# Kernel optimization log

Hardware: AMD Instinct MI355X
Metric: run time of the kernel (lower is better)

Reference implementation:

```python
import jax, jax.numpy as jnp
import numpy as np

N_NODES = 100000
N_EDGES = 1250000
IN_CH = 128
OUT_CH = 64


def setup_inputs() -> dict:
    key = jax.random.key(0)
    k1, k2, k3, k4 = jax.random.split(key, 4)
    x = jax.random.normal(k1, (N_NODES, IN_CH), dtype=jnp.float32)
    edge_index = jax.random.randint(k2, (2, N_EDGES), 0, N_NODES, dtype=jnp.int64)
    edge_weight = jax.random.uniform(k3, (N_EDGES,), dtype=jnp.float32)
    # Xavier-uniform weight, zero bias (as in reset_parameters)
    limit = float(np.sqrt(6.0 / (IN_CH + OUT_CH)))
    W = jax.random.uniform(k4, (IN_CH, OUT_CH), dtype=jnp.float32, minval=-limit, maxval=limit)
    b = jnp.zeros((OUT_CH,), dtype=jnp.float32)
    return {"x": x, "edge_index": edge_index, "edge_weight": edge_weight, "W": W, "b": b}


def reference(x, edge_index, edge_weight, W, b):
    # Dense transform: [N, in] @ [in, out] -> [N, out]
    h = jnp.matmul(x, W)
    row, col = edge_index[0], edge_index[1]
    n = h.shape[0]
    # Weighted in-degree via scatter-add on destination (row)
    deg = jnp.zeros((n,), dtype=h.dtype).at[row].add(edge_weight)
    # deg^-0.5 with inf (deg==0) replaced by 0
    deg_inv_sqrt = jnp.where(deg == 0, jnp.zeros_like(deg), deg ** -0.5)
    norm = deg_inv_sqrt[row] * deg_inv_sqrt[col]  # [E]
    # Gather source features, normalize, scatter-add to destinations
    out = jnp.zeros_like(h).at[row].add(h[col] * norm[:, None])
    return out + b
```

## Files before the change

kernel.cpp:

```cpp
#include <hip/hip_runtime.h>

#define N_NODES 100000
#define N_EDGES 1250000
#define IN_CH 128
#define OUT_CH 64

#define NPB 128
#define ACCS2 33
#define NBINS 782
#define BINCAP_DEF 2048
#define NB1 256
#define B1T 512
#define CH1 ((N_EDGES + NB1 - 1) / NB1)
#define MAXU ((CH1 + B1T - 1) / B1T)
#define CURS_STRIDE 16

#define QSCALE 8192.0f
#define QBIAS_F 16777216.0f
#define QBIAS_U 16777216u
#define INV_QSCALE 1.220703125e-4f
#define SCALE_DEG 33554432.0f
#define INV_SCALE_DEG 2.9802322387695312e-08f

typedef __attribute__((ext_vector_type(8))) short short8;
typedef __attribute__((ext_vector_type(4))) float f32x4;

__device__ inline unsigned int f2bf(float f) {
    unsigned int u = __float_as_uint(f);
    unsigned int r = ((u >> 16) & 1u) + 0x7FFFu;
    return (u + r) >> 16;
}
__device__ inline float bf_lo(unsigned int p) { return __uint_as_float(p << 16); }
__device__ inline float bf_hi(unsigned int p) { return __uint_as_float(p & 0xFFFF0000u); }

__device__ inline unsigned long long qpack(unsigned int p) {
    unsigned int lo = (unsigned int)__float2int_rn(fmaf(bf_lo(p), QSCALE, QBIAS_F));
    unsigned int hi = (unsigned int)__float2int_rn(fmaf(bf_hi(p), QSCALE, QBIAS_F));
    return ((unsigned long long)hi << 32) | (unsigned long long)lo;
}

__global__ __launch_bounds__(256) void wbconv_kernel(const float* __restrict__ W,
                                                     unsigned int* __restrict__ Wb,
                                                     int* __restrict__ cursor,
                                                     int bincap) {
    int g = blockIdx.x * 256 + threadIdx.x;
    if (g < NBINS) cursor[g * CURS_STRIDE] = g * bincap;

    int c = g >> 8;
    int t = (g >> 6) & 3;
    int l = g & 63;
    int q = l >> 4, r15 = l & 15;
    unsigned int o[4];
#pragma unroll
    for (int jj = 0; jj < 4; ++jj) {
        float f0 = W[(c * 32 + q * 8 + 2 * jj)     * OUT_CH + t * 16 + r15];
        float f1 = W[(c * 32 + q * 8 + 2 * jj + 1) * OUT_CH + t * 16 + r15];
        o[jj] = f2bf(f0) | (f2bf(f1) << 16);
    }
    *(uint4*)(Wb + (size_t)g * 4) = make_uint4(o[0], o[1], o[2], o[3]);
}

__global__ __launch_bounds__(B1T) void bin1_kernel(const int* __restrict__ ei,
                                                   const float* __restrict__ ew,
                                                   int* __restrict__ cursor,
                                                   int2* __restrict__ brec,
                                                   int bincap) {
    __shared__ int hist[NBINS];
    __shared__ int base[NBINS];
    __shared__ int rank[NBINS];
    const int t = threadIdx.x;
    for (int i = t; i < NBINS; i += B1T) { hist[i] = 0; rank[i] = 0; }
    __syncthreads();

    const int e0 = blockIdx.x * CH1;
    const int e1 = (e0 + CH1 < N_EDGES) ? e0 + CH1 : N_EDGES;

    int rowv[MAXU], colv[MAXU];
    float wv[MAXU];
#pragma unroll
    for (int u = 0; u < MAXU; ++u) {
        int e = e0 + t + u * B1T;
        bool ok = e < e1;
        rowv[u] = ok ? ei[e] : -1;
        colv[u] = ok ? ei[N_EDGES + e] : 0;
        wv[u]   = ok ? ew[e] : 0.0f;
        if (ok) atomicAdd(&hist[rowv[u] >> 7], 1);
    }
    __syncthreads();

    for (int i = t; i < NBINS; i += B1T)
        if (hist[i] > 0) base[i] = atomicAdd(&cursor[i * CURS_STRIDE], hist[i]);
    __syncthreads();

#pragma unroll
    for (int u = 0; u < MAXU; ++u) {
        if (rowv[u] >= 0) {
            int b = rowv[u] >> 7;
            int rk = atomicAdd(&rank[b], 1);
            int idx = base[b] + rk;
            if (idx < (b + 1) * bincap)
                brec[idx] = make_int2(((rowv[u] & 127) << 17) | colv[u],
                                      __float_as_int(wv[u]));
        }
    }
}

__global__ __launch_bounds__(256) void bin2_kernel(const int* __restrict__ cursor,
                                                   const int2* __restrict__ brec,
                                                   float* __restrict__ dis_g,
                                                   int bincap) {
    __shared__ int deg[NPB];
    const int t = threadIdx.x;
    const int b = blockIdx.x;
    if (t < NPB) deg[t] = 0;
    __syncthreads();

    const int rbase = b * bincap;
    int m = cursor[b * CURS_STRIDE] - rbase;
    if (m > bincap) m = bincap;

    for (int j = t; j < m; j += 256) {
        int2 rec = brec[rbase + j];
        atomicAdd(&deg[rec.x >> 17], __float2int_rn(__int_as_float(rec.y) * SCALE_DEG));
    }
    __syncthreads();

    int node = b * NPB + t;
    if (t < NPB && node < N_NODES) {
        float d = (float)deg[t] * INV_SCALE_DEG;
        dis_g[node] = (d == 0.0f) ? 0.0f : (1.0f / sqrtf(d));
    }
}

__global__ __launch_bounds__(256) void gemm_kernel(const float* __restrict__ x,
                                                   const unsigned int* __restrict__ Wb,
                                                   const float* __restrict__ dis,
                                                   unsigned int* __restrict__ hs) {
    const int tid  = threadIdx.x;
    const int w    = tid >> 6;
    const int lane = tid & 63;
    const int q    = lane >> 4, r15 = lane & 15;
    const int node = blockIdx.x * 64 + w * 16 + r15;
    const int nl   = (node < N_NODES) ? node : N_NODES - 1;
    const float* xrow = x + (size_t)nl * IN_CH;

    f32x4 acc[4];
#pragma unroll
    for (int t = 0; t < 4; ++t) acc[t] = (f32x4){0.f, 0.f, 0.f, 0.f};

#pragma unroll
    for (int c = 0; c < 4; ++c) {
        float4 xa = *(const float4*)(xrow + c * 32 + q * 8);
        float4 xb = *(const float4*)(xrow + c * 32 + q * 8 + 4);
        short8 bfrag;
        bfrag[0] = (short)f2bf(xa.x); bfrag[1] = (short)f2bf(xa.y);
        bfrag[2] = (short)f2bf(xa.z); bfrag[3] = (short)f2bf(xa.w);
        bfrag[4] = (short)f2bf(xb.x); bfrag[5] = (short)f2bf(xb.y);
        bfrag[6] = (short)f2bf(xb.z); bfrag[7] = (short)f2bf(xb.w);
#pragma unroll
        for (int t = 0; t < 4; ++t) {
            short8 afrag = *(const short8*)(Wb + (size_t)((c * 4 + t) * 64 + lane) * 4);
            acc[t] = __builtin_amdgcn_mfma_f32_16x16x32_bf16(afrag, bfrag, acc[t], 0, 0, 0);
        }
    }

    if (node < N_NODES) {
        float di = dis[node];
#pragma unroll
        for (int t = 0; t < 4; ++t) {
            unsigned int p0 = f2bf(acc[t][0] * di) | (f2bf(acc[t][1] * di) << 16);
            unsigned int p1 = f2bf(acc[t][2] * di) | (f2bf(acc[t][3] * di) << 16);
            *(uint2*)(hs + (size_t)node * 32 + t * 8 + q * 2) = make_uint2(p0, p1);
        }
    }
}

__global__ __launch_bounds__(512) void bingather_kernel(const int* __restrict__ cursor,
                                                        const int2* __restrict__ brec,
                                                        const uint4* __restrict__ hs,
                                                        const float* __restrict__ dis,
                                                        const float* __restrict__ b,
                                                        float* __restrict__ out,
                                                        int bincap) {
    __shared__ unsigned long long acc[NPB * ACCS2];
    __shared__ int cnt[NPB];
    const int t = threadIdx.x;
    const int blk = blockIdx.x;
    for (int k = t; k < NPB * ACCS2; k += 512) acc[k] = 0ull;
    if (t < NPB) cnt[t] = 0;
    __syncthreads();

    const int rbase = blk * bincap;
    int m = cursor[blk * CURS_STRIDE] - rbase;
    if (m > bincap) m = bincap;

    const int wid = t >> 6, lane = t & 63;
    const int sub = lane >> 3, l8 = lane & 7;

    for (int j0 = wid * 16; j0 < m; j0 += 128) {
        int jA = j0 + sub;
        int jB = j0 + 8 + sub;
        bool okA = jA < m, okB = jB < m;
        int recA = okA ? brec[rbase + jA].x : 0;
        int recB = okB ? brec[rbase + jB].x : 0;
        uint4 pA = make_uint4(0, 0, 0, 0), pB = make_uint4(0, 0, 0, 0);
        if (okA) pA = hs[(size_t)(recA & 0x1FFFF) * 8 + l8];
        if (okB) pB = hs[(size_t)(recB & 0x1FFFF) * 8 + l8];
        if (okA) {
            int ba = (recA >> 17) * ACCS2 + 4 * l8;
            atomicAdd(&acc[ba + 0], qpack(pA.x));
            atomicAdd(&acc[ba + 1], qpack(pA.y));
            atomicAdd(&acc[ba + 2], qpack(pA.z));
            atomicAdd(&acc[ba + 3], qpack(pA.w));
            if (l8 == 0) atomicAdd(&cnt[recA >> 17], 1);
        }
        if (okB) {
            int bb = (recB >> 17) * ACCS2 + 4 * l8;
            atomicAdd(&acc[bb + 0], qpack(pB.x));
            atomicAdd(&acc[bb + 1], qpack(pB.y));
            atomicAdd(&acc[bb + 2], qpack(pB.z));
            atomicAdd(&acc[bb + 3], qpack(pB.w));
            if (l8 == 0) atomicAdd(&cnt[recB >> 17], 1);
        }
    }
    __syncthreads();

    const unsigned int* acc32 = (const unsigned int*)acc;
    float bc = b[lane];
    int half = lane & 1, slot = lane >> 1;
#pragma unroll 4
    for (int r = 0; r < 16; ++r) {
        int nl = wid * 16 + r;
        int node = blk * NPB + nl;
        if (node < N_NODES) {
            unsigned int raw = acc32[(nl * ACCS2 + slot) * 2 + half];
            int qsum = (int)(raw - (unsigned int)cnt[nl] * QBIAS_U);
            float di = dis[node] * INV_QSCALE;
            out[(size_t)node * OUT_CH + lane] = (float)qsum * di + bc;
        }
    }
}

extern "C" void kernel_launch(void* const* d_in, const int* in_sizes, int n_in,
                              void* d_out, int out_size, void* d_ws, size_t ws_size,
                              hipStream_t stream) {
    const float* x  = (const float*)d_in[0];
    const int*   ei = (const int*)d_in[1];
    const float* ew = (const float*)d_in[2];
    const float* W  = (const float*)d_in[3];
    const float* b  = (const float*)d_in[4];
    float* out = (float*)d_out;

    unsigned int* hs = (unsigned int*)d_ws;
    unsigned int* Wb = hs + (size_t)N_NODES * 32;
    int*   cursor  = (int*)(Wb + 4096);
    float* dis     = (float*)(cursor + NBINS * CURS_STRIDE);
    int2*  brec    = (int2*)(dis + N_NODES);
    size_t used = (size_t)N_NODES * 32 + 4096 + (size_t)NBINS * CURS_STRIDE
                + (size_t)N_NODES;
    size_t rem  = (ws_size / 4 > used) ? ws_size / 4 - used : 0;
    int bincap  = (int)(rem / (2 * (size_t)NBINS));
    if (bincap > BINCAP_DEF) bincap = BINCAP_DEF;

    wbconv_kernel<<<4, 256, 0, stream>>>(W, Wb, cursor, bincap);
    bin1_kernel<<<NB1, B1T, 0, stream>>>(ei, ew, cursor, brec, bincap);
    bin2_kernel<<<NBINS, 256, 0, stream>>>(cursor, brec, dis, bincap);
    gemm_kernel<<<(N_NODES + 63) / 64, 256, 0, stream>>>(x, Wb, dis, hs);
    bingather_kernel<<<NBINS, 512, 0, stream>>>(cursor, brec, (const uint4*)hs,
                                                dis, b, out, bincap);
}
```

Measured before the change: 164.5 us.

## Fuse binning and GEMM into one launch, compute degree via global atomics

Merges the edge-binning pass and the dense bf16 MFMA transform into one kernel, with separate blocks doing each job so they run concurrently. The separate degree kernel is dropped: weighted degree is accumulated with global integer atomics during binning, and the source-side normalisation moves into the gather, where each edge looks up the source degree and takes rsqrt. Edge records shrink from 8 to 4 bytes because the weight is no longer stored, and the quantisation bias is halved. The trade is many global atomics on the degree array plus an extra degree load and rsqrt per edge in the gather.

```diff
diff --git a/kernel.cpp b/kernel.cpp
--- a/kernel.cpp
+++ b/kernel.cpp
@@ -14,10 +14,11 @@
 #define CH1 ((N_EDGES + NB1 - 1) / NB1)
 #define MAXU ((CH1 + B1T - 1) / B1T)
 #define CURS_STRIDE 16
+#define GEMM_BLOCKS ((N_NODES + 127) / 128)
 
 #define QSCALE 8192.0f
-#define QBIAS_F 16777216.0f
-#define QBIAS_U 16777216u
+#define QBIAS_F 8388608.0f
+#define QBIAS_U 8388608u
 #define INV_QSCALE 1.220703125e-4f
 #define SCALE_DEG 33554432.0f
 #define INV_SCALE_DEG 2.9802322387695312e-08f
@@ -33,193 +34,175 @@
 __device__ inline float bf_lo(unsigned int p) { return __uint_as_float(p << 16); }
 __device__ inline float bf_hi(unsigned int p) { return __uint_as_float(p & 0xFFFF0000u); }
 
-__device__ inline unsigned long long qpack(unsigned int p) {
-    unsigned int lo = (unsigned int)__float2int_rn(fmaf(bf_lo(p), QSCALE, QBIAS_F));
-    unsigned int hi = (unsigned int)__float2int_rn(fmaf(bf_hi(p), QSCALE, QBIAS_F));
+__device__ inline unsigned long long qpacks(unsigned int p, float sc) {
+    unsigned int lo = (unsigned int)__float2int_rn(fmaf(bf_lo(p), sc, QBIAS_F));
+    unsigned int hi = (unsigned int)__float2int_rn(fmaf(bf_hi(p), sc, QBIAS_F));
     return ((unsigned long long)hi << 32) | (unsigned long long)lo;
 }
 
-__global__ __launch_bounds__(256) void wbconv_kernel(const float* __restrict__ W,
-                                                     unsigned int* __restrict__ Wb,
-                                                     int* __restrict__ cursor,
-                                                     int bincap) {
+__global__ __launch_bounds__(256) void init_kernel(const float* __restrict__ W,
+                                                   unsigned int* __restrict__ Wb,
+                                                   int* __restrict__ cursor,
+                                                   int* __restrict__ deg,
+                                                   int bincap) {
     int g = blockIdx.x * 256 + threadIdx.x;
     if (g < NBINS) cursor[g * CURS_STRIDE] = g * bincap;
-
-    int c = g >> 8;
-    int t = (g >> 6) & 3;
-    int l = g & 63;
-    int q = l >> 4, r15 = l & 15;
-    unsigned int o[4];
-#pragma unroll
-    for (int jj = 0; jj < 4; ++jj) {
-        float f0 = W[(c * 32 + q * 8 + 2 * jj)     * OUT_CH + t * 16 + r15];
-        float f1 = W[(c * 32 + q * 8 + 2 * jj + 1) * OUT_CH + t * 16 + r15];
-        o[jj] = f2bf(f0) | (f2bf(f1) << 16);
-    }
-    *(uint4*)(Wb + (size_t)g * 4) = make_uint4(o[0], o[1], o[2], o[3]);
-}
-
-__global__ __launch_bounds__(B1T) void bin1_kernel(const int* __restrict__ ei,
-                                                   const float* __restrict__ ew,
-                                                   int* __restrict__ cursor,
-                                                   int2* __restrict__ brec,
-                                                   int bincap) {
+    if (g < 25000) *(uint4*)(deg + g * 4) = make_uint4(0u, 0u, 0u, 0u);
+    if (g < 1024) {
+        int c = g >> 8;
+        int t4 = (g >> 6) & 3;
+        int l = g & 63;
+        int q = l >> 4, r15 = l & 15;
+        unsigned int o[4];
+#pragma unroll
+        for (int jj = 0; jj < 4; ++jj) {
+            float f0 = W[(c * 32 + q * 8 + 2 * jj)     * OUT_CH + t4 * 16 + r15];
+            float f1 = W[(c * 32 + q * 8 + 2 * jj + 1) * OUT_CH + t4 * 16 + r15];
+            o[jj] = f2bf(f0) | (f2bf(f1) << 16);
+        }
+        *(uint4*)(Wb + (size_t)g * 4) = make_uint4(o[0], o[1], o[2], o[3]);
+    }
+}
+
+__global__ __launch_bounds__(512) void fused_kernel(const float* __restrict__ x,
+                                                    const unsigned int* __restrict__ Wb,
+                                                    const int* __restrict__ ei,
+                                                    const float* __restrict__ ew,
+                                                    int* __restrict__ cursor,
+                                                    int* __restrict__ deg,
+                                                    int* __restrict__ brec,
+                                                    unsigned int* __restrict__ hs,
+                                                    int bincap) {
     __shared__ int hist[NBINS];
     __shared__ int base[NBINS];
     __shared__ int rank[NBINS];
-    const int t = threadIdx.x;
-    for (int i = t; i < NBINS; i += B1T) { hist[i] = 0; rank[i] = 0; }
-    __syncthreads();
-
-    const int e0 = blockIdx.x * CH1;
-    const int e1 = (e0 + CH1 < N_EDGES) ? e0 + CH1 : N_EDGES;
-
-    int rowv[MAXU], colv[MAXU];
-    float wv[MAXU];
-#pragma unroll
-    for (int u = 0; u < MAXU; ++u) {
-        int e = e0 + t + u * B1T;
-        bool ok = e < e1;
-        rowv[u] = ok ? ei[e] : -1;
-        colv[u] = ok ? ei[N_EDGES + e] : 0;
-        wv[u]   = ok ? ew[e] : 0.0f;
-        if (ok) atomicAdd(&hist[rowv[u] >> 7], 1);
-    }
-    __syncthreads();
-
-    for (int i = t; i < NBINS; i += B1T)
-        if (hist[i] > 0) base[i] = atomicAdd(&cursor[i * CURS_STRIDE], hist[i]);
-    __syncthreads();
-
-#pragma unroll
-    for (int u = 0; u < MAXU; ++u) {
-        if (rowv[u] >= 0) {
-            int b = rowv[u] >> 7;
-            int rk = atomicAdd(&rank[b], 1);
-            int idx = base[b] + rk;
-            if (idx < (b + 1) * bincap)
-                brec[idx] = make_int2(((rowv[u] & 127) << 17) | colv[u],
-                                      __float_as_int(wv[u]));
-        }
-    }
-}
-
-__global__ __launch_bounds__(256) void bin2_kernel(const int* __restrict__ cursor,
-                                                   const int2* __restrict__ brec,
-                                                   float* __restrict__ dis_g,
-                                                   int bincap) {
-    __shared__ int deg[NPB];
-    const int t = threadIdx.x;
-    const int b = blockIdx.x;
-    if (t < NPB) deg[t] = 0;
-    __syncthreads();
-
-    const int rbase = b * bincap;
-    int m = cursor[b * CURS_STRIDE] - rbase;
-    if (m > bincap) m = bincap;
-
-    for (int j = t; j < m; j += 256) {
-        int2 rec = brec[rbase + j];
-        atomicAdd(&deg[rec.x >> 17], __float2int_rn(__int_as_float(rec.y) * SCALE_DEG));
-    }
-    __syncthreads();
-
-    int node = b * NPB + t;
-    if (t < NPB && node < N_NODES) {
-        float d = (float)deg[t] * INV_SCALE_DEG;
-        dis_g[node] = (d == 0.0f) ? 0.0f : (1.0f / sqrtf(d));
-    }
-}
-
-__global__ __launch_bounds__(256) void gemm_kernel(const float* __restrict__ x,
-                                                   const unsigned int* __restrict__ Wb,
-                                                   const float* __restrict__ dis,
-                                                   unsigned int* __restrict__ hs) {
-    const int tid  = threadIdx.x;
-    const int w    = tid >> 6;
-    const int lane = tid & 63;
-    const int q    = lane >> 4, r15 = lane & 15;
-    const int node = blockIdx.x * 64 + w * 16 + r15;
-    const int nl   = (node < N_NODES) ? node : N_NODES - 1;
-    const float* xrow = x + (size_t)nl * IN_CH;
-
-    f32x4 acc[4];
-#pragma unroll
-    for (int t = 0; t < 4; ++t) acc[t] = (f32x4){0.f, 0.f, 0.f, 0.f};
-
-#pragma unroll
-    for (int c = 0; c < 4; ++c) {
-        float4 xa = *(const float4*)(xrow + c * 32 + q * 8);
-        float4 xb = *(const float4*)(xrow + c * 32 + q * 8 + 4);
-        short8 bfrag;
-        bfrag[0] = (short)f2bf(xa.x); bfrag[1] = (short)f2bf(xa.y);
-        bfrag[2] = (short)f2bf(xa.z); bfrag[3] = (short)f2bf(xa.w);
-        bfrag[4] = (short)f2bf(xb.x); bfrag[5] = (short)f2bf(xb.y);
-        bfrag[6] = (short)f2bf(xb.z); bfrag[7] = (short)f2bf(xb.w);
-#pragma unroll
-        for (int t = 0; t < 4; ++t) {
-            short8 afrag = *(const short8*)(Wb + (size_t)((c * 4 + t) * 64 + lane) * 4);
-            acc[t] = __builtin_amdgcn_mfma_f32_16x16x32_bf16(afrag, bfrag, acc[t], 0, 0, 0);
-        }
-    }
-
-    if (node < N_NODES) {
-        float di = dis[node];
-#pragma unroll
-        for (int t = 0; t < 4; ++t) {
-            unsigned int p0 = f2bf(acc[t][0] * di) | (f2bf(acc[t][1] * di) << 16);
-            unsigned int p1 = f2bf(acc[t][2] * di) | (f2bf(acc[t][3] * di) << 16);
-            *(uint2*)(hs + (size_t)node * 32 + t * 8 + q * 2) = make_uint2(p0, p1);
-        }
-    }
-}
-
-__global__ __launch_bounds__(512) void bingather_kernel(const int* __restrict__ cursor,
-                                                        const int2* __restrict__ brec,
-                                                        const uint4* __restrict__ hs,
-                                                        const float* __restrict__ dis,
-                                                        const float* __restrict__ b,
-                                                        float* __restrict__ out,
-                                                        int bincap) {
+    const int tid = threadIdx.x;
+
+    if (blockIdx.x < NB1) {
+        for (int i = tid; i < NBINS; i += B1T) { hist[i] = 0; rank[i] = 0; }
+        __syncthreads();
+
+        const int e0 = blockIdx.x * CH1;
+        const int e1 = (e0 + CH1 < N_EDGES) ? e0 + CH1 : N_EDGES;
+
+        int rowv[MAXU], colv[MAXU];
+#pragma unroll
+        for (int u = 0; u < MAXU; ++u) {
+            int e = e0 + tid + u * B1T;
+            bool ok = e < e1;
+            rowv[u] = ok ? ei[e] : -1;
+            colv[u] = ok ? ei[N_EDGES + e] : 0;
+            if (ok) {
+                float wgt = ew[e];
+                atomicAdd(&hist[rowv[u] >> 7], 1);
+                atomicAdd(&deg[rowv[u]], __float2int_rn(wgt * SCALE_DEG));
+            }
+        }
+        __syncthreads();
+
+        for (int i = tid; i < NBINS; i += B1T)
+            if (hist[i] > 0) base[i] = atomicAdd(&cursor[i * CURS_STRIDE], hist[i]);
+        __syncthreads();
+
+#pragma unroll
+        for (int u = 0; u < MAXU; ++u) {
+            if (rowv[u] >= 0) {
+                int bb = rowv[u] >> 7;
+                int rk = atomicAdd(&rank[bb], 1);
+                int idx = base[bb] + rk;
+                if (idx < (bb + 1) * bincap)
+                    brec[idx] = ((rowv[u] & 127) << 17) | colv[u];
+            }
+        }
+    } else {
+        const int blk  = blockIdx.x - NB1;
+        const int w    = tid >> 6;
+        const int lane = tid & 63;
+        const int q    = lane >> 4, r15 = lane & 15;
+        const int node = blk * 128 + w * 16 + r15;
+        const int nl   = (node < N_NODES) ? node : N_NODES - 1;
+        const float* xrow = x + (size_t)nl * IN_CH;
+
+        f32x4 acc[4];
+#pragma unroll
+        for (int t = 0; t < 4; ++t) acc[t] = (f32x4){0.f, 0.f, 0.f, 0.f};
+
+#pragma unroll
+        for (int c = 0; c < 4; ++c) {
+            float4 xa = *(const float4*)(xrow + c * 32 + q * 8);
+            float4 xb = *(const float4*)(xrow + c * 32 + q * 8 + 4);
+            short8 bfrag;
+            bfrag[0] = (short)f2bf(xa.x); bfrag[1] = (short)f2bf(xa.y);
+            bfrag[2] = (short)f2bf(xa.z); bfrag[3] = (short)f2bf(xa.w);
+            bfrag[4] = (short)f2bf(xb.x); bfrag[5] = (short)f2bf(xb.y);
+            bfrag[6] = (short)f2bf(xb.z); bfrag[7] = (short)f2bf(xb.w);
+#pragma unroll
+            for (int t = 0; t < 4; ++t) {
+                short8 afrag = *(const short8*)(Wb + (size_t)((c * 4 + t) * 64 + lane) * 4);
+                acc[t] = __builtin_amdgcn_mfma_f32_16x16x32_bf16(afrag, bfrag, acc[t], 0, 0, 0);
+            }
+        }
+
+        if (node < N_NODES) {
+#pragma unroll
+            for (int t = 0; t < 4; ++t) {
+                unsigned int p0 = f2bf(acc[t][0]) | (f2bf(acc[t][1]) << 16);
+                unsigned int p1 = f2bf(acc[t][2]) | (f2bf(acc[t][3]) << 16);
+                *(uint2*)(hs + (size_t)node * 32 + t * 8 + q * 2) = make_uint2(p0, p1);
+            }
+        }
+    }
+}
+
+__global__ __launch_bounds__(512) void gather_kernel(const int* __restrict__ cursor,
+                                                     const int* __restrict__ brec,
+                                                     const uint4* __restrict__ hs,
+                                                     const int* __restrict__ deg,
+                                                     const float* __restrict__ b,
+                                                     float* __restrict__ out,
+                                                     int bincap) {
     __shared__ unsigned long long acc[NPB * ACCS2];
     __shared__ int cnt[NPB];
-    const int t = threadIdx.x;
+    const int tid = threadIdx.x;
     const int blk = blockIdx.x;
-    for (int k = t; k < NPB * ACCS2; k += 512) acc[k] = 0ull;
-    if (t < NPB) cnt[t] = 0;
+    for (int k = tid; k < NPB * ACCS2; k += 512) acc[k] = 0ull;
+    if (tid < NPB) cnt[tid] = 0;
     __syncthreads();
 
     const int rbase = blk * bincap;
     int m = cursor[blk * CURS_STRIDE] - rbase;
     if (m > bincap) m = bincap;
 
-    const int wid = t >> 6, lane = t & 63;
+    const int wid = tid >> 6, lane = tid & 63;
     const int sub = lane >> 3, l8 = lane & 7;
 
     for (int j0 = wid * 16; j0 < m; j0 += 128) {
         int jA = j0 + sub;
         int jB = j0 + 8 + sub;
         bool okA = jA < m, okB = jB < m;
-        int recA = okA ? brec[rbase + jA].x : 0;
-        int recB = okB ? brec[rbase + jB].x : 0;
+        int recA = okA ? brec[rbase + jA] : 0;
+        int recB = okB ? brec[rbase + jB] : 0;
         uint4 pA = make_uint4(0, 0, 0, 0), pB = make_uint4(0, 0, 0, 0);
         if (okA) pA = hs[(size_t)(recA & 0x1FFFF) * 8 + l8];
         if (okB) pB = hs[(size_t)(recB & 0x1FFFF) * 8 + l8];
         if (okA) {
+            float d  = (float)deg[recA & 0x1FFFF] * INV_SCALE_DEG;
+            float sc = (d == 0.0f) ? 0.0f : QSCALE * rsqrtf(d);
             int ba = (recA >> 17) * ACCS2 + 4 * l8;
-            atomicAdd(&acc[ba + 0], qpack(pA.x));
-            atomicAdd(&acc[ba + 1], qpack(pA.y));
-            atomicAdd(&acc[ba + 2], qpack(pA.z));
-            atomicAdd(&acc[ba + 3], qpack(pA.w));
+            atomicAdd(&acc[ba + 0], qpacks(pA.x, sc));
+            atomicAdd(&acc[ba + 1], qpacks(pA.y, sc));
+            atomicAdd(&acc[ba + 2], qpacks(pA.z, sc));
+            atomicAdd(&acc[ba + 3], qpacks(pA.w, sc));
             if (l8 == 0) atomicAdd(&cnt[recA >> 17], 1);
         }
         if (okB) {
+            float d  = (float)deg[recB & 0x1FFFF] * INV_SCALE_DEG;
+            float sc = (d == 0.0f) ? 0.0f : QSCALE * rsqrtf(d);
             int bb = (recB >> 17) * ACCS2 + 4 * l8;
-            atomicAdd(&acc[bb + 0], qpack(pB.x));
-            atomicAdd(&acc[bb + 1], qpack(pB.y));
-            atomicAdd(&acc[bb + 2], qpack(pB.z));
-            atomicAdd(&acc[bb + 3], qpack(pB.w));
+            atomicAdd(&acc[bb + 0], qpacks(pB.x, sc));
+            atomicAdd(&acc[bb + 1], qpacks(pB.y, sc));
+            atomicAdd(&acc[bb + 2], qpacks(pB.z, sc));
+            atomicAdd(&acc[bb + 3], qpacks(pB.w, sc));
             if (l8 == 0) atomicAdd(&cnt[recB >> 17], 1);
         }
     }
@@ -235,8 +218,9 @@
         if (node < N_NODES) {
             unsigned int raw = acc32[(nl * ACCS2 + slot) * 2 + half];
             int qsum = (int)(raw - (unsigned int)cnt[nl] * QBIAS_U);
-            float di = dis[node] * INV_QSCALE;
-            out[(size_t)node * OUT_CH + lane] = (float)qsum * di + bc;
+            float dr = (float)deg[node] * INV_SCALE_DEG;
+            float di = (dr == 0.0f) ? 0.0f : (1.0f / sqrtf(dr));
+            out[(size_t)node * OUT_CH + lane] = (float)qsum * (di * INV_QSCALE) + bc;
         }
     }
 }
@@ -253,19 +237,18 @@
 
     unsigned int* hs = (unsigned int*)d_ws;
     unsigned int* Wb = hs + (size_t)N_NODES * 32;
-    int*   cursor  = (int*)(Wb + 4096);
-    float* dis     = (float*)(cursor + NBINS * CURS_STRIDE);
-    int2*  brec    = (int2*)(dis + N_NODES);
+    int* cursor = (int*)(Wb + 4096);
+    int* deg    = cursor + NBINS * CURS_STRIDE;
+    int* brec   = deg + N_NODES;
     size_t used = (size_t)N_NODES * 32 + 4096 + (size_t)NBINS * CURS_STRIDE
                 + (size_t)N_NODES;
     size_t rem  = (ws_size / 4 > used) ? ws_size / 4 - used : 0;
-    int bincap  = (int)(rem / (2 * (size_t)NBINS));
+    int bincap  = (int)(rem / (size_t)NBINS);
     if (bincap > BINCAP_DEF) bincap = BINCAP_DEF;
 
-    wbconv_kernel<<<4, 256, 0, stream>>>(W, Wb, cursor, bincap);
-    bin1_kernel<<<NB1, B1T, 0, stream>>>(ei, ew, cursor, brec, bincap);
-    bin2_kernel<<<NBINS, 256, 0, stream>>>(cursor, brec, dis, bincap);
-    gemm_kernel<<<(N_NODES + 63) / 64, 256, 0, stream>>>(x, Wb, dis, hs);
-    bingather_kernel<<<NBINS, 512, 0, stream>>>(cursor, brec, (const uint4*)hs,
-                                                dis, b, out, bincap);
-}
+    init_kernel<<<98, 256, 0, stream>>>(W, Wb, cursor, deg, bincap);
+    fused_kernel<<<NB1 + GEMM_BLOCKS, 512, 0, stream>>>(x, Wb, ei, ew, cursor, deg,
+                                                        brec, hs, bincap);
+    gather_kernel<<<NBINS, 512, 0, stream>>>(cursor, brec, (const uint4*)hs,
+                                             deg, b, out, bincap);
+}
```

After: 210.0 us. 27.6% more time.
